# Optimization experiments

Measured on AMD Instinct MI355X. Metric: run time of the kernel, lower is better.

The kernel has to match this reference:

```python
import jax, jax.numpy as jnp
import numpy as np

B, N, H, E = 16, 1024, 256, 16384
NUM_LAYERS = 4


def setup_inputs() -> dict:
    key = jax.random.key(0)
    ks = jax.random.split(key, 7)
    embedding = jax.random.normal(ks[0], (B, N, H), dtype=jnp.float32)
    edge_idx = jax.random.randint(ks[1], (2, E), 0, N, dtype=jnp.int64 if jax.config.jax_enable_x64 else jnp.int32)
    weight = jax.random.normal(ks[2], (NUM_LAYERS, H, H), dtype=jnp.float32) * 0.05
    w_ih = jax.random.normal(ks[3], (3 * H, H), dtype=jnp.float32) * 0.05
    w_hh = jax.random.normal(ks[4], (3 * H, H), dtype=jnp.float32) * 0.05
    b_ih = jax.random.normal(ks[5], (3 * H,), dtype=jnp.float32) * 0.05
    b_hh = jax.random.normal(ks[6], (3 * H,), dtype=jnp.float32) * 0.05
    return {"embedding": embedding, "edge_idx": edge_idx, "weight": weight,
            "w_ih": w_ih, "w_hh": w_hh, "b_ih": b_ih, "b_hh": b_hh}


def _gru_cell(inp, h, w_ih, w_hh, b_ih, b_hh):
    # torch.nn.GRUCell math: gates packed as [r, z, n]
    gi = inp @ w_ih.T + b_ih   # [B, N, 3H]
    gh = h @ w_hh.T + b_hh     # [B, N, 3H]
    i_r, i_z, i_n = jnp.split(gi, 3, axis=-1)
    h_r, h_z, h_n = jnp.split(gh, 3, axis=-1)
    r = jax.nn.sigmoid(i_r + h_r)
    z = jax.nn.sigmoid(i_z + h_z)
    n = jnp.tanh(i_n + r * h_n)
    return (1.0 - z) * n + z * h


def reference(embedding, edge_idx, weight, w_ih, w_hh, b_ih, b_hh):
    # GatedGraphConv(out_channels=H, num_layers=4, aggr='add') applied to a
    # batch of disjoint graphs sharing the same edge structure. Instead of
    # flattening nodes with batch offsets (as the torch code does), we keep
    # the [B, N, H] layout and scatter along the node axis - identical math.
    src = edge_idx[0]  # message source (x_j)
    dst = edge_idx[1]  # aggregation target
    x = embedding  # embedding_dim == hidden_dim, no zero-padding needed
    num_layers = weight.shape[0]
    for l in range(num_layers):
        m = jnp.einsum('bnh,hk->bnk', x, weight[l])          # [B, N, H]
        msg = m[:, src, :]                                    # gather [B, E, H]
        agg = jnp.zeros_like(x).at[:, dst, :].add(msg)        # scatter-add
        x = _gru_cell(agg, x, w_ih, w_hh, b_ih, b_hh)
    return x  # [B, N, H]
```

## Files before the change

### kernel.cpp

```cpp
#include <hip/hip_runtime.h>
#include <hip/hip_bf16.h>

typedef _Float16 f16;
typedef _Float16 f16x4 __attribute__((ext_vector_type(4)));
typedef _Float16 f16x8 __attribute__((ext_vector_type(8)));
typedef float f32x4 __attribute__((ext_vector_type(4)));

#define NB 16
#define NN 1024
#define HH 256
#define NE 16384
#define NL 4
#define NM (NB * NN)


__global__ void cvt_f32_f16(const float* __restrict__ s, f16* __restrict__ d, int n) {
    int i = blockIdx.x * 256 + threadIdx.x;
    if (i < n) d[i] = (f16)s[i];
}

__global__ void cvt_f32_f16v(const float* __restrict__ s, f16* __restrict__ d, int n8) {
    int i = blockIdx.x * 256 + threadIdx.x;
    if (i < n8) {
        const float4* p = (const float4*)(s + (size_t)i * 8);
        float4 a = p[0], b = p[1];
        f16x8 v;
        v[0] = (f16)a.x; v[1] = (f16)a.y; v[2] = (f16)a.z; v[3] = (f16)a.w;
        v[4] = (f16)b.x; v[5] = (f16)b.y; v[6] = (f16)b.z; v[7] = (f16)b.w;
        *(f16x8*)(d + (size_t)i * 8) = v;
    }
}

__global__ void zero_i32(int* p, int n) {
    int i = blockIdx.x * 256 + threadIdx.x;
    if (i < n) p[i] = 0;
}

__global__ void hist_kernel(const int* __restrict__ dst, int* cnt) {
    int e = blockIdx.x * 256 + threadIdx.x;
    if (e < NE) atomicAdd(&cnt[dst[e]], 1);
}

__global__ __launch_bounds__(1024) void scan_kernel(const int* __restrict__ cnt,
                                                    int* __restrict__ offs,
                                                    int* __restrict__ cur) {
    __shared__ int s[1024];
    int i = threadIdx.x;
    int c = cnt[i];
    s[i] = c;
    __syncthreads();
    for (int ofs = 1; ofs < 1024; ofs <<= 1) {
        int v = (i >= ofs) ? s[i - ofs] : 0;
        __syncthreads();
        s[i] += v;
        __syncthreads();
    }
    offs[i + 1] = s[i];
    if (i == 0) offs[0] = 0;
    cur[i] = s[i] - c;
}

__global__ void fill_kernel(const int* __restrict__ src, const int* __restrict__ dst,
                            int* cur, int* __restrict__ ssrc) {
    int e = blockIdx.x * 256 + threadIdx.x;
    if (e < NE) {
        int pos = atomicAdd(&cur[dst[e]], 1);
        ssrc[pos] = src[e];
    }
}

__global__ __launch_bounds__(256) void wct_gemm(const f16* __restrict__ wih,
                                                const f16* __restrict__ wl,
                                                f16* __restrict__ wct) {
    int wid = threadIdx.x >> 6, lane = threadIdx.x & 63;
    int tile = blockIdx.x * 4 + wid;
    int l = tile / 768, rem = tile % 768;
    int jt = rem / 16, ht = rem % 16;
    const f16* A = wih + (size_t)(jt * 16 + (lane & 15)) * 256 + (lane >> 4) * 8;
    const f16* B = wl + (size_t)l * 65536 + (size_t)(ht * 16 + (lane & 15)) * 256 + (lane >> 4) * 8;
    f32x4 acc;
    for (int r = 0; r < 4; ++r) acc[r] = 0.f;
    for (int k = 0; k < 256; k += 32) {
        f16x8 a = *(const f16x8*)(A + k);
        f16x8 b = *(const f16x8*)(B + k);
        acc = __builtin_amdgcn_mfma_f32_16x16x32_f16(a, b, acc, 0, 0, 0);
    }
    int col = lane & 15, row0 = (lane >> 4) * 4;
    for (int r = 0; r < 4; ++r)
        wct[(size_t)l * 196608 + (size_t)(jt * 16 + row0 + r) * 256 + ht * 16 + col] = (f16)acc[r];
}

__global__ __launch_bounds__(256) void agg_f16(const f16* __restrict__ xh,
                                               const int* __restrict__ offs,
                                               const int* __restrict__ ssrc,
                                               f16* __restrict__ ab) {
    int bid = blockIdx.x;
    int b = (bid & 7) + ((bid >> 11) << 3);
    int n = ((bid >> 3) & 255) * 4 + (threadIdx.x >> 6);
    int lane = threadIdx.x & 63;
    const f16* xb = xh + ((size_t)b << 18);
    int e0 = offs[n], e1 = offs[n + 1];
    float s0 = 0.f, s1 = 0.f, s2 = 0.f, s3 = 0.f;
    int p = e0;
    for (; p + 1 < e1; p += 2) {
        int i0 = ssrc[p], i1 = ssrc[p + 1];
        f16x4 v0 = *(const f16x4*)(xb + (((size_t)i0) << 8) + lane * 4);
        f16x4 v1 = *(const f16x4*)(xb + (((size_t)i1) << 8) + lane * 4);
        s0 += (float)v0[0] + (float)v1[0];
        s1 += (float)v0[1] + (float)v1[1];
        s2 += (float)v0[2] + (float)v1[2];
        s3 += (float)v0[3] + (float)v1[3];
    }
    if (p < e1) {
        f16x4 v0 = *(const f16x4*)(xb + (((size_t)ssrc[p]) << 8) + lane * 4);
        s0 += (float)v0[0]; s1 += (float)v0[1]; s2 += (float)v0[2]; s3 += (float)v0[3];
    }
    int row = (b << 10) + n;
    f16x4 o; o[0] = (f16)s0; o[1] = (f16)s1; o[2] = (f16)s2; o[3] = (f16)s3;
    *(f16x4*)(ab + (size_t)row * 256 + lane * 4) = o;
}

__global__ __launch_bounds__(256) void agg_f32(const float* __restrict__ x,
                                               const int* __restrict__ offs,
                                               const int* __restrict__ ssrc,
                                               f16* __restrict__ ab) {
    int row = blockIdx.x * 4 + (threadIdx.x >> 6);
    int lane = threadIdx.x & 63;
    int b = row >> 10, n = row & 1023;
    int e0 = offs[n], e1 = offs[n + 1];
    float s0 = 0.f, s1 = 0.f, s2 = 0.f, s3 = 0.f;
    const float* xb = x + ((size_t)b << 18);
    for (int p = e0; p < e1; ++p) {
        float4 v = *(const float4*)(xb + (((size_t)ssrc[p]) << 8) + lane * 4);
        s0 += v.x; s1 += v.y; s2 += v.z; s3 += v.w;
    }
    f16x4 o; o[0] = (f16)s0; o[1] = (f16)s1; o[2] = (f16)s2; o[3] = (f16)s3;
    *(f16x4*)(ab + (size_t)row * 512 + lane * 4) = o;
    float4 v = *(const float4*)(x + (size_t)row * 256 + lane * 4);
    f16x4 o2; o2[0] = (f16)v.x; o2[1] = (f16)v.y; o2[2] = (f16)v.z; o2[3] = (f16)v.w;
    *(f16x4*)(ab + (size_t)row * 512 + 256 + lane * 4) = o2;
}

__global__ __launch_bounds__(256) void gemm_gru_v8(const f16* __restrict__ ab,
                                                   const f16* __restrict__ xh,
                                                   const f16* __restrict__ wct,
                                                   const f16* __restrict__ whh,
                                                   const float* __restrict__ bih,
                                                   const float* __restrict__ bhh,
                                                   float* __restrict__ out,
                                                   f16* __restrict__ xh_dst,
                                                   int wout, int wxh) {
    __shared__ __align__(16) f16 Ay[64 * 32];
    __shared__ __align__(16) f16 Ax[64 * 32];
    __shared__ __align__(16) f16 Bs[192 * 32];

    const int tid = threadIdx.x;
    const int w = tid >> 6, lane = tid & 63;
    const int fr = lane & 15, sg = lane >> 4;
    const int m0 = blockIdx.x * 64;
    const int j0 = blockIdx.y * 32;

    const int rA = tid >> 2, cA = tid & 3;
    const f16* gy = ab + (size_t)(m0 + rA) * 256 + cA * 8;
    const f16* gx = xh + (size_t)(m0 + rA) * 256 + cA * 8;
    const int wA = rA * 32 + ((cA ^ ((rA >> 1) & 3)) * 8);
    const f16 *gb0, *gb1, *gb2;
    int wB0, wB1, wB2;
    {
        int u0 = tid, u1 = tid + 256, u2 = tid + 512;
        int rr0 = u0 >> 2, rr1 = u1 >> 2, rr2 = u2 >> 2;
        int g0 = rr0 >> 5, g1 = rr1 >> 5, g2 = rr2 >> 5;
        gb0 = ((g0 < 3) ? (wct + (size_t)(g0 * 256 + j0 + (rr0 & 31)) * 256)
                        : (whh + (size_t)((g0 - 3) * 256 + j0 + (rr0 & 31)) * 256)) + (u0 & 3) * 8;
        gb1 = ((g1 < 3) ? (wct + (size_t)(g1 * 256 + j0 + (rr1 & 31)) * 256)
                        : (whh + (size_t)((g1 - 3) * 256 + j0 + (rr1 & 31)) * 256)) + (u1 & 3) * 8;
        gb2 = ((g2 < 3) ? (wct + (size_t)(g2 * 256 + j0 + (rr2 & 31)) * 256)
                        : (whh + (size_t)((g2 - 3) * 256 + j0 + (rr2 & 31)) * 256)) + (u2 & 3) * 8;
        wB0 = rr0 * 32 + (((u0 & 3) ^ ((rr0 >> 1) & 3)) * 8);
        wB1 = rr1 * 32 + (((u1 & 3) ^ ((rr1 >> 1) & 3)) * 8);
        wB2 = rr2 * 32 + (((u2 & 3) ^ ((rr2 >> 1) & 3)) * 8);
    }

    int aoff;
    {
        int row = w * 16 + fr;
        aoff = row * 32 + ((sg ^ ((row >> 1) & 3)) * 8);
    }
    int boff[6][2];
#pragma unroll
    for (int g = 0; g < 6; ++g)
#pragma unroll
        for (int jt = 0; jt < 2; ++jt) {
            int row = g * 32 + jt * 16 + fr;
            boff[g][jt] = row * 32 + ((sg ^ ((row >> 1) & 3)) * 8);
        }

    f32x4 acc[6][2];
#pragma unroll
    for (int g = 0; g < 6; ++g)
#pragma unroll
        for (int jt = 0; jt < 2; ++jt)
#pragma unroll
            for (int r = 0; r < 4; ++r) acc[g][jt][r] = 0.f;

    f16x8 ry, rx, rb0, rb1, rb2;
#define LOADREGS(KK)                          \
    do {                                      \
        ry = *(const f16x8*)(gy + (KK));      \
        rx = *(const f16x8*)(gx + (KK));      \
        rb0 = *(const f16x8*)(gb0 + (KK));    \
        rb1 = *(const f16x8*)(gb1 + (KK));    \
        rb2 = *(const f16x8*)(gb2 + (KK));    \
    } while (0)

    LOADREGS(0);

#pragma unroll
    for (int t = 0; t < 8; ++t) {
        if (t) __syncthreads();
        *(f16x8*)(Ay + wA) = ry;
        *(f16x8*)(Ax + wA) = rx;
        *(f16x8*)(Bs + wB0) = rb0;
        *(f16x8*)(Bs + wB1) = rb1;
        *(f16x8*)(Bs + wB2) = rb2;
        __syncthreads();
        if (t < 7) LOADREGS((t + 1) * 32);

        f16x8 aY = *(const f16x8*)(Ay + aoff);
        f16x8 aX = *(const f16x8*)(Ax + aoff);
#pragma unroll
        for (int g = 0; g < 6; ++g) {
#pragma unroll
            for (int jt = 0; jt < 2; ++jt) {
                f16x8 bF = *(const f16x8*)(Bs + boff[g][jt]);
                acc[g][jt] = __builtin_amdgcn_mfma_f32_16x16x32_f16(
                    (g < 3) ? aY : aX, bF, acc[g][jt], 0, 0, 0);
            }
        }
    }
#undef LOADREGS

#pragma unroll
    for (int jt = 0; jt < 2; ++jt) {
        int j = j0 + jt * 16 + fr;
        float bir = bih[j], biz = bih[j + 256], bin = bih[j + 512];
        float bhr = bhh[j], bhz = bhh[j + 256], bhn = bhh[j + 512];
#pragma unroll
        for (int r = 0; r < 4; ++r) {
            int row = m0 + w * 16 + sg * 4 + r;
            float gir = acc[0][jt][r] + bir;
            float giz = acc[1][jt][r] + biz;
            float gin = acc[2][jt][r] + bin;
            float ghr = acc[3][jt][r] + bhr;
            float ghz = acc[4][jt][r] + bhz;
            float ghn = acc[5][jt][r] + bhn;
            float rg = 1.f / (1.f + __expf(-(gir + ghr)));
            float zg = 1.f / (1.f + __expf(-(giz + ghz)));
            float ng = tanhf(gin + rg * ghn);
            float h = (float)xh[(size_t)row * 256 + j];
            float res = (1.f - zg) * ng + zg * h;
            if (wout) out[(size_t)row * 256 + j] = res;
            if (wxh) xh_dst[(size_t)row * 256 + j] = (f16)res;
        }
    }
}

__global__ __launch_bounds__(256) void gemm_gru_slow(const f16* __restrict__ ab,
                                                     const f16* __restrict__ wct,
                                                     const f16* __restrict__ whh,
                                                     const float* __restrict__ bih,
                                                     const float* __restrict__ bhh,
                                                     const float* __restrict__ x_src,
                                                     float* __restrict__ out) {
    __shared__ __align__(16) f16 As[2][64][40];
    __shared__ __align__(16) f16 Bs[6][32][40];

    int m0 = blockIdx.x * 64;
    int j0 = blockIdx.y * 32;
    int tid = threadIdx.x;
    int wid = tid >> 6, lane = tid & 63;

    f32x4 acc[6][2];
#pragma unroll
    for (int g = 0; g < 6; ++g)
#pragma unroll
        for (int jt = 0; jt < 2; ++jt)
#pragma unroll
            for (int r = 0; r < 4; ++r) acc[g][jt][r] = 0.f;

    int ar = tid >> 2, ac = (tid & 3) * 8;

    for (int kk = 0; kk < 256; kk += 32) {
        f16x8 a0 = *(const f16x8*)(ab + (size_t)(m0 + ar) * 512 + kk + ac);
        f16x8 a1 = *(const f16x8*)(ab + (size_t)(m0 + ar) * 512 + 256 + kk + ac);
        *(f16x8*)(&As[0][ar][ac]) = a0;
        *(f16x8*)(&As[1][ar][ac]) = a1;
#pragma unroll
        for (int i = 0; i < 3; ++i) {
            int idx = tid + i * 256;
            int g = idx >> 7;
            int r = (idx >> 2) & 31;
            int c = (idx & 3) * 8;
            const f16* src = (g < 3)
                ? (wct + (size_t)(j0 + g * 256 + r) * 256 + kk + c)
                : (whh + (size_t)(j0 + (g - 3) * 256 + r) * 256 + kk + c);
            *(f16x8*)(&Bs[g][r][c]) = *(const f16x8*)src;
        }
        __syncthreads();

        int fr = lane & 15, fo = (lane >> 4) * 8;
        f16x8 aF[2];
        aF[0] = *(const f16x8*)(&As[0][wid * 16 + fr][fo]);
        aF[1] = *(const f16x8*)(&As[1][wid * 16 + fr][fo]);
#pragma unroll
        for (int g = 0; g < 6; ++g) {
#pragma unroll
            for (int jt = 0; jt < 2; ++jt) {
                f16x8 bF = *(const f16x8*)(&Bs[g][jt * 16 + fr][fo]);
                acc[g][jt] = __builtin_amdgcn_mfma_f32_16x16x32_f16(
                    (g < 3) ? aF[0] : aF[1], bF, acc[g][jt], 0, 0, 0);
            }
        }
        __syncthreads();
    }

    int fr = lane & 15, frow = (lane >> 4) * 4;
#pragma unroll
    for (int jt = 0; jt < 2; ++jt) {
        int j = j0 + jt * 16 + fr;
        float bir = bih[j], biz = bih[j + 256], bin = bih[j + 512];
        float bhr = bhh[j], bhz = bhh[j + 256], bhn = bhh[j + 512];
#pragma unroll
        for (int r = 0; r < 4; ++r) {
            int row = m0 + wid * 16 + frow + r;
            float gir = acc[0][jt][r] + bir;
            float giz = acc[1][jt][r] + biz;
            float gin = acc[2][jt][r] + bin;
            float ghr = acc[3][jt][r] + bhr;
            float ghz = acc[4][jt][r] + bhz;
            float ghn = acc[5][jt][r] + bhn;
            float rg = 1.f / (1.f + __expf(-(gir + ghr)));
            float zg = 1.f / (1.f + __expf(-(giz + ghz)));
            float ng = tanhf(gin + rg * ghn);
            float h = x_src[(size_t)row * 256 + j];
            out[(size_t)row * 256 + j] = (1.f - zg) * ng + zg * h;
        }
    }
}


extern "C" void kernel_launch(void* const* d_in, const int* in_sizes, int n_in,
                              void* d_out, int out_size, void* d_ws, size_t ws_size,
                              hipStream_t stream) {
    const float* emb = (const float*)d_in[0];
    const int* eidx = (const int*)d_in[1];
    const float* W = (const float*)d_in[2];
    const float* wih = (const float*)d_in[3];
    const float* whh = (const float*)d_in[4];
    const float* bih = (const float*)d_in[5];
    const float* bhh = (const float*)d_in[6];
    float* out = (float*)d_out;

    const size_t NEL = (size_t)NM * 256;
    f16* ab = (f16*)d_ws;
    f16* xhA = ab + NEL;
    f16* xhB = xhA + NEL;
    f16* wct_f = xhB + NEL;
    const size_t need = ((size_t)3 * NEL + 786432 + 196608 + 196608 + 262144) * 2 + 80000;
    bool fast = ws_size >= need;

    f16 *wct, *whh_h, *wih_h, *w_h;
    if (fast) {
        wct = wct_f;
    } else {
        wct = (f16*)((char*)d_ws + (size_t)16 * 1024 * 1024);
    }
    whh_h = wct + (size_t)4 * 768 * 256;
    wih_h = whh_h + (size_t)768 * 256;
    w_h = wih_h + (size_t)768 * 256;
    int* cnt = (int*)(w_h + (size_t)4 * 256 * 256);
    int* offs = cnt + 1024;
    int* cur = offs + 1056;
    int* ssrc = cur + 1024;

    cvt_f32_f16<<<(768 * 256 + 255) / 256, 256, 0, stream>>>(wih, wih_h, 768 * 256);
    cvt_f32_f16<<<(768 * 256 + 255) / 256, 256, 0, stream>>>(whh, whh_h, 768 * 256);
    cvt_f32_f16<<<(4 * 256 * 256 + 255) / 256, 256, 0, stream>>>(W, w_h, 4 * 256 * 256);

    zero_i32<<<4, 256, 0, stream>>>(cnt, 1024);
    hist_kernel<<<64, 256, 0, stream>>>(eidx + NE, cnt);
    scan_kernel<<<1, 1024, 0, stream>>>(cnt, offs, cur);
    fill_kernel<<<64, 256, 0, stream>>>(eidx, eidx + NE, cur, ssrc);

    wct_gemm<<<768, 256, 0, stream>>>(wih_h, w_h, wct);

    if (fast) {
        cvt_f32_f16v<<<(int)(NEL / 8 + 255) / 256, 256, 0, stream>>>(emb, xhA, (int)(NEL / 8));
        for (int l = 0; l < NL; ++l) {
            f16* xs = (l & 1) ? xhB : xhA;
            f16* xd = (l & 1) ? xhA : xhB;
            agg_f16<<<NM / 4, 256, 0, stream>>>(xs, offs, ssrc, ab);
            gemm_gru_v8<<<dim3(NM / 64, 8), 256, 0, stream>>>(
                ab, xs, wct + (size_t)l * 768 * 256, whh_h, bih, bhh,
                out, xd, (l == NL - 1) ? 1 : 0, (l < NL - 1) ? 1 : 0);
        }
    } else {
        const float* xs = emb;
        for (int l = 0; l < NL; ++l) {
            agg_f32<<<NM / 4, 256, 0, stream>>>(xs, offs, ssrc, ab);
            gemm_gru_slow<<<dim3(NM / 64, 8), 256, 0, stream>>>(
                ab, wct + (size_t)l * 768 * 256, whh_h, bih, bhh, xs, out);
            xs = out;
        }
    }
}
```

Measured before the change: 231.2 us.

## Switch GRU GEMM to 32x32x16 MFMA with 128-row tiles and merged gate accumulators

The fused GEMM+GRU kernel moves from 16x16x32 MFMA to 32x32x16 MFMA and doubles the M tile from 64 to 128 rows per block, so each wave covers 32 rows. The r and z gate contributions from the input and hidden paths now accumulate into a single accumulator each, with biases pre-loaded into the accumulators. This cuts accumulator count, LDS fragment reads per FLOP and epilogue adds. In exchange the grid is half as large and each thread uses more LDS and registers, which may reduce occupancy.

After: 233.6 us. Within noise of the previous version (+1.0%).

```diff
diff --git a/kernel.cpp b/kernel.cpp
--- a/kernel.cpp
+++ b/kernel.cpp
@@ -5,6 +5,7 @@
 typedef _Float16 f16x4 __attribute__((ext_vector_type(4)));
 typedef _Float16 f16x8 __attribute__((ext_vector_type(8)));
 typedef float f32x4 __attribute__((ext_vector_type(4)));
+typedef float f32x16 __attribute__((ext_vector_type(16)));
 
 #define NB 16
 #define NN 1024
@@ -141,7 +142,7 @@
     *(f16x4*)(ab + (size_t)row * 512 + 256 + lane * 4) = o2;
 }
 
-__global__ __launch_bounds__(256) void gemm_gru_v8(const f16* __restrict__ ab,
+__global__ __launch_bounds__(256) void gemm_gru_v9(const f16* __restrict__ ab,
                                                    const f16* __restrict__ xh,
                                                    const f16* __restrict__ wct,
                                                    const f16* __restrict__ whh,
@@ -150,20 +151,24 @@
                                                    float* __restrict__ out,
                                                    f16* __restrict__ xh_dst,
                                                    int wout, int wxh) {
-    __shared__ __align__(16) f16 Ay[64 * 32];
-    __shared__ __align__(16) f16 Ax[64 * 32];
+    __shared__ __align__(16) f16 Ay[128 * 32];
+    __shared__ __align__(16) f16 Ax[128 * 32];
     __shared__ __align__(16) f16 Bs[192 * 32];
 
     const int tid = threadIdx.x;
     const int w = tid >> 6, lane = tid & 63;
-    const int fr = lane & 15, sg = lane >> 4;
-    const int m0 = blockIdx.x * 64;
+    const int col = lane & 31, kh = lane >> 5;
+    const int m0 = blockIdx.x * 128;
     const int j0 = blockIdx.y * 32;
 
-    const int rA = tid >> 2, cA = tid & 3;
-    const f16* gy = ab + (size_t)(m0 + rA) * 256 + cA * 8;
-    const f16* gx = xh + (size_t)(m0 + rA) * 256 + cA * 8;
-    const int wA = rA * 32 + ((cA ^ ((rA >> 1) & 3)) * 8);
+    const int rA0 = tid >> 2, cA = tid & 3;
+    const int rA1 = rA0 + 64;
+    const f16* gy0 = ab + (size_t)(m0 + rA0) * 256 + cA * 8;
+    const f16* gy1 = ab + (size_t)(m0 + rA1) * 256 + cA * 8;
+    const f16* gx0 = xh + (size_t)(m0 + rA0) * 256 + cA * 8;
+    const f16* gx1 = xh + (size_t)(m0 + rA1) * 256 + cA * 8;
+    const int wA0 = rA0 * 32 + ((cA ^ ((rA0 >> 1) & 3)) * 8);
+    const int wA1 = rA1 * 32 + ((cA ^ ((rA1 >> 1) & 3)) * 8);
     const f16 *gb0, *gb1, *gb2;
     int wB0, wB1, wB2;
     {
@@ -181,36 +186,42 @@
         wB2 = rr2 * 32 + (((u2 & 3) ^ ((rr2 >> 1) & 3)) * 8);
     }
 
-    int aoff;
+    int aoff[2], boff[6][2];
+#pragma unroll
+    for (int mk = 0; mk < 2; ++mk) {
+        int row = w * 32 + col;
+        int ch = mk * 2 + kh;
+        aoff[mk] = row * 32 + ((ch ^ ((row >> 1) & 3)) * 8);
+#pragma unroll
+        for (int g = 0; g < 6; ++g) {
+            int br = g * 32 + col;
+            boff[g][mk] = br * 32 + ((ch ^ ((br >> 1) & 3)) * 8);
+        }
+    }
+
+    const int j = j0 + col;
+    f32x16 acc[4];
     {
-        int row = w * 16 + fr;
-        aoff = row * 32 + ((sg ^ ((row >> 1) & 3)) * 8);
-    }
-    int boff[6][2];
-#pragma unroll
-    for (int g = 0; g < 6; ++g)
-#pragma unroll
-        for (int jt = 0; jt < 2; ++jt) {
-            int row = g * 32 + jt * 16 + fr;
-            boff[g][jt] = row * 32 + ((sg ^ ((row >> 1) & 3)) * 8);
-        }
-
-    f32x4 acc[6][2];
-#pragma unroll
-    for (int g = 0; g < 6; ++g)
-#pragma unroll
-        for (int jt = 0; jt < 2; ++jt)
-#pragma unroll
-            for (int r = 0; r < 4; ++r) acc[g][jt][r] = 0.f;
-
-    f16x8 ry, rx, rb0, rb1, rb2;
-#define LOADREGS(KK)                          \
-    do {                                      \
-        ry = *(const f16x8*)(gy + (KK));      \
-        rx = *(const f16x8*)(gx + (KK));      \
-        rb0 = *(const f16x8*)(gb0 + (KK));    \
-        rb1 = *(const f16x8*)(gb1 + (KK));    \
-        rb2 = *(const f16x8*)(gb2 + (KK));    \
+        float br = bih[j] + bhh[j];
+        float bz = bih[j + 256] + bhh[j + 256];
+        float bn1 = bih[j + 512];
+        float bn2 = bhh[j + 512];
+#pragma unroll
+        for (int q = 0; q < 16; ++q) {
+            acc[0][q] = br; acc[1][q] = bz; acc[2][q] = bn1; acc[3][q] = bn2;
+        }
+    }
+
+    f16x8 ry0, ry1, rx0, rx1, rb0, rb1, rb2;
+#define LOADREGS(KK)                           \
+    do {                                       \
+        ry0 = *(const f16x8*)(gy0 + (KK));     \
+        ry1 = *(const f16x8*)(gy1 + (KK));     \
+        rx0 = *(const f16x8*)(gx0 + (KK));     \
+        rx1 = *(const f16x8*)(gx1 + (KK));     \
+        rb0 = *(const f16x8*)(gb0 + (KK));     \
+        rb1 = *(const f16x8*)(gb1 + (KK));     \
+        rb2 = *(const f16x8*)(gb2 + (KK));     \
     } while (0)
 
     LOADREGS(0);
@@ -218,50 +229,46 @@
 #pragma unroll
     for (int t = 0; t < 8; ++t) {
         if (t) __syncthreads();
-        *(f16x8*)(Ay + wA) = ry;
-        *(f16x8*)(Ax + wA) = rx;
+        *(f16x8*)(Ay + wA0) = ry0;
+        *(f16x8*)(Ay + wA1) = ry1;
+        *(f16x8*)(Ax + wA0) = rx0;
+        *(f16x8*)(Ax + wA1) = rx1;
         *(f16x8*)(Bs + wB0) = rb0;
         *(f16x8*)(Bs + wB1) = rb1;
         *(f16x8*)(Bs + wB2) = rb2;
         __syncthreads();
         if (t < 7) LOADREGS((t + 1) * 32);
 
-        f16x8 aY = *(const f16x8*)(Ay + aoff);
-        f16x8 aX = *(const f16x8*)(Ax + aoff);
-#pragma unroll
-        for (int g = 0; g < 6; ++g) {
-#pragma unroll
-            for (int jt = 0; jt < 2; ++jt) {
-                f16x8 bF = *(const f16x8*)(Bs + boff[g][jt]);
-                acc[g][jt] = __builtin_amdgcn_mfma_f32_16x16x32_f16(
-                    (g < 3) ? aY : aX, bF, acc[g][jt], 0, 0, 0);
-            }
+#pragma unroll
+        for (int mk = 0; mk < 2; ++mk) {
+            f16x8 aY = *(const f16x8*)(Ay + aoff[mk]);
+            f16x8 aX = *(const f16x8*)(Ax + aoff[mk]);
+            f16x8 b0 = *(const f16x8*)(Bs + boff[0][mk]);
+            f16x8 b1 = *(const f16x8*)(Bs + boff[1][mk]);
+            f16x8 b2 = *(const f16x8*)(Bs + boff[2][mk]);
+            f16x8 b3 = *(const f16x8*)(Bs + boff[3][mk]);
+            f16x8 b4 = *(const f16x8*)(Bs + boff[4][mk]);
+            f16x8 b5 = *(const f16x8*)(Bs + boff[5][mk]);
+            acc[0] = __builtin_amdgcn_mfma_f32_32x32x16_f16(aY, b0, acc[0], 0, 0, 0);
+            acc[1] = __builtin_amdgcn_mfma_f32_32x32x16_f16(aY, b1, acc[1], 0, 0, 0);
+            acc[2] = __builtin_amdgcn_mfma_f32_32x32x16_f16(aY, b2, acc[2], 0, 0, 0);
+            acc[0] = __builtin_amdgcn_mfma_f32_32x32x16_f16(aX, b3, acc[0], 0, 0, 0);
+            acc[1] = __builtin_amdgcn_mfma_f32_32x32x16_f16(aX, b4, acc[1], 0, 0, 0);
+            acc[3] = __builtin_amdgcn_mfma_f32_32x32x16_f16(aX, b5, acc[3], 0, 0, 0);
         }
     }
 #undef LOADREGS
 
 #pragma unroll
-    for (int jt = 0; jt < 2; ++jt) {
-        int j = j0 + jt * 16 + fr;
-        float bir = bih[j], biz = bih[j + 256], bin = bih[j + 512];
-        float bhr = bhh[j], bhz = bhh[j + 256], bhn = bhh[j + 512];
-#pragma unroll
-        for (int r = 0; r < 4; ++r) {
-            int row = m0 + w * 16 + sg * 4 + r;
-            float gir = acc[0][jt][r] + bir;
-            float giz = acc[1][jt][r] + biz;
-            float gin = acc[2][jt][r] + bin;
-            float ghr = acc[3][jt][r] + bhr;
-            float ghz = acc[4][jt][r] + bhz;
-            float ghn = acc[5][jt][r] + bhn;
-            float rg = 1.f / (1.f + __expf(-(gir + ghr)));
-            float zg = 1.f / (1.f + __expf(-(giz + ghz)));
-            float ng = tanhf(gin + rg * ghn);
-            float h = (float)xh[(size_t)row * 256 + j];
-            float res = (1.f - zg) * ng + zg * h;
-            if (wout) out[(size_t)row * 256 + j] = res;
-            if (wxh) xh_dst[(size_t)row * 256 + j] = (f16)res;
-        }
+    for (int q = 0; q < 16; ++q) {
+        int row = m0 + w * 32 + (q & 3) + 8 * (q >> 2) + 4 * kh;
+        float rg = 1.f / (1.f + __expf(-acc[0][q]));
+        float zg = 1.f / (1.f + __expf(-acc[1][q]));
+        float ng = tanhf(acc[2][q] + rg * acc[3][q]);
+        float h = (float)xh[(size_t)row * 256 + j];
+        float res = (1.f - zg) * ng + zg * h;
+        if (wout) out[(size_t)row * 256 + j] = res;
+        if (wxh) xh_dst[(size_t)row * 256 + j] = (f16)res;
     }
 }
 
@@ -400,7 +407,7 @@
             f16* xs = (l & 1) ? xhB : xhA;
             f16* xd = (l & 1) ? xhA : xhB;
             agg_f16<<<NM / 4, 256, 0, stream>>>(xs, offs, ssrc, ab);
-            gemm_gru_v8<<<dim3(NM / 64, 8), 256, 0, stream>>>(
+            gemm_gru_v9<<<dim3(NM / 128, 8), 256, 0, stream>>>(
                 ab, xs, wct + (size_t)l * 768 * 256, whh_h, bih, bhh,
                 out, xd, (l == NL - 1) ? 1 : 0, (l < NL - 1) ? 1 : 0);
         }
```
